# Optimization experiments

Measured on AMD Instinct MI355X. Metric: run time of the kernel, lower is better.

The kernel has to match this reference:

```python
import jax, jax.numpy as jnp
import numpy as np

N, E, ND, ED, H1, H2 = 50000, 800000, 128, 16, 256, 32
NEG_SLOPE = 0.2


def setup_inputs() -> dict:
    key = jax.random.key(0)
    ks = jax.random.split(key, 12)
    s = lambda k, shape: jax.random.normal(k, shape, jnp.float32) * 0.05
    return dict(
        x=jax.random.normal(ks[0], (N, ND), jnp.float32),
        edge_index=jax.random.randint(ks[1], (2, E), 0, N),
        edge_attr=jax.random.normal(ks[2], (E, ED), jnp.float32),
        Wl1=s(ks[3], (H1, ND)), bl1=jnp.zeros((H1,), jnp.float32),
        Wr1=s(ks[4], (H1, ND)), br1=jnp.zeros((H1,), jnp.float32),
        We1=s(ks[5], (H1, ED)), att1=s(ks[6], (H1,)), bias1=jnp.zeros((H1,), jnp.float32),
        Wl2=s(ks[7], (H2, H1)), bl2=jnp.zeros((H2,), jnp.float32),
        Wr2=s(ks[8], (H2, H1)), br2=jnp.zeros((H2,), jnp.float32),
        We2=s(ks[9], (H2, ED)), att2=s(ks[10], (H2,)), bias2=jnp.zeros((H2,), jnp.float32),
    )


def _gatv2_layer(x, src, dst, ea, Wl, bl, Wr, br, We, att, bias, n):
    # heads=1, concat=True  (PyG GATv2Conv defaults)
    xl = x @ Wl.T + bl                      # [n, C]  source transform
    xr = x @ Wr.T + br                      # [n, C]  target transform
    # per-edge message: x_j + x_i + lin_edge(edge_attr), then LeakyReLU
    m = jax.nn.leaky_relu(xl[src] + xr[dst] + ea @ We.T, NEG_SLOPE)  # [Etot, C]
    logit = m @ att                         # [Etot]
    # segment softmax over destination nodes (numerically stable)
    lmax = jax.ops.segment_max(logit, dst, num_segments=n)
    lmax = jnp.where(jnp.isfinite(lmax), lmax, 0.0)
    a = jnp.exp(logit - lmax[dst])
    denom = jax.ops.segment_sum(a, dst, num_segments=n)
    a = a / denom[dst]                      # self-loops guarantee denom > 0
    # scatter-add of alpha-weighted source features, plus output bias
    return jax.ops.segment_sum(xl[src] * a[:, None], dst, num_segments=n) + bias


def reference(x, edge_index, edge_attr,
              Wl1, bl1, Wr1, br1, We1, att1, bias1,
              Wl2, bl2, Wr2, br2, We2, att2, bias2):
    n = x.shape[0]
    src, dst = edge_index[0], edge_index[1]
    # add_self_loops=True with fill_value='mean': loop attr = mean incoming edge_attr
    deg = jax.ops.segment_sum(jnp.ones_like(dst, jnp.float32), dst, num_segments=n)
    loop_attr = jax.ops.segment_sum(edge_attr, dst, num_segments=n) / jnp.maximum(deg, 1.0)[:, None]
    loop = jnp.arange(n)
    src_f = jnp.concatenate([src, loop])
    dst_f = jnp.concatenate([dst, loop])
    ea = jnp.concatenate([edge_attr, loop_attr], axis=0)
    h = _gatv2_layer(x, src_f, dst_f, ea, Wl1, bl1, Wr1, br1, We1, att1, bias1, n)
    h = _gatv2_layer(h, src_f, dst_f, ea, Wl2, bl2, Wr2, br2, We2, att2, bias2, n)
    return h.mean(axis=0)  # [out_dim]
```

## Files before the change

kernel.cpp:

```cpp
#include <hip/hip_runtime.h>
#include <math.h>

#define N_NODES 50000
#define N_EDGES 800000
#define ND 128
#define ED 16
#define H1 256
#define H2 32

typedef short bf16x8 __attribute__((ext_vector_type(8)));
typedef float f32x4 __attribute__((ext_vector_type(4)));
typedef _Float16 half2v __attribute__((ext_vector_type(2)));

__device__ __forceinline__ float dot2h(uint a, uint b, float c) {
    asm("v_dot2_f32_f16 %0, %1, %2, %0" : "+v"(c) : "v"(a), "v"(b));
    return c;
}
__device__ __forceinline__ float fmamix_lo(uint a, float b, float c) {
    float d;
    asm("v_fma_mix_f32 %0, %1, %2, %3 op_sel_hi:[1,0,0]" : "=v"(d) : "v"(a), "v"(b), "v"(c));
    return d;
}
__device__ __forceinline__ float fmamix_hi(uint a, float b, float c) {
    float d;
    asm("v_fma_mix_f32 %0, %1, %2, %3 op_sel:[1,0,0] op_sel_hi:[1,0,0]" : "=v"(d) : "v"(a), "v"(b), "v"(c));
    return d;
}
__device__ __forceinline__ ushort f2bf(float f) {
    uint u = __float_as_uint(f);
    return (ushort)((u + 0x7fff + ((u >> 16) & 1)) >> 16);
}

__global__ void k_deg(const int* __restrict__ ei, int* __restrict__ counts, int E) {
    int e = blockIdx.x * blockDim.x + threadIdx.x;
    if (e < E) atomicAdd(&counts[ei[E + e]], 1);
}

__global__ void k_scan1(const int* __restrict__ counts, int* __restrict__ partial, int n, int chunk) {
    __shared__ int sh[256];
    int beg = blockIdx.x * chunk, end = min(beg + chunk, n);
    int sum = 0;
    for (int i = beg + threadIdx.x; i < end; i += 256) sum += counts[i] + 1;
    sh[threadIdx.x] = sum;
    __syncthreads();
    for (int off = 128; off; off >>= 1) {
        if (threadIdx.x < off) sh[threadIdx.x] += sh[threadIdx.x + off];
        __syncthreads();
    }
    if (threadIdx.x == 0) partial[blockIdx.x] = sh[0];
}
__global__ void k_scan2(int* __restrict__ partial) {
    __shared__ int sh[256];
    int v = partial[threadIdx.x];
    sh[threadIdx.x] = v;
    __syncthreads();
    for (int off = 1; off < 256; off <<= 1) {
        int t = (threadIdx.x >= off) ? sh[threadIdx.x - off] : 0;
        __syncthreads();
        sh[threadIdx.x] += t;
        __syncthreads();
    }
    partial[threadIdx.x] = sh[threadIdx.x] - v;
}
__global__ void k_scan3(const int* __restrict__ counts, const int* __restrict__ partial,
                        int* __restrict__ rowptr, int n, int chunk) {
    __shared__ int sh[256];
    int beg = blockIdx.x * chunk, end = min(beg + chunk, n);
    int run = partial[blockIdx.x];
    for (int base = beg; base < end; base += 256) {
        int i = base + threadIdx.x;
        int v = (i < end) ? counts[i] + 1 : 0;
        sh[threadIdx.x] = v;
        __syncthreads();
        for (int off = 1; off < 256; off <<= 1) {
            int t = (threadIdx.x >= off) ? sh[threadIdx.x - off] : 0;
            __syncthreads();
            sh[threadIdx.x] += t;
            __syncthreads();
        }
        if (i < end) rowptr[i + 1] = run + sh[threadIdx.x];
        __syncthreads();
        run += sh[255];
        __syncthreads();
    }
    if (blockIdx.x == 0 && threadIdx.x == 0) rowptr[0] = 0;
}

__global__ void k_fill_csr(const int* __restrict__ ei, const float* __restrict__ ea,
                           const int* __restrict__ rowptr, int* __restrict__ fill,
                           int* __restrict__ csr_src, _Float16* __restrict__ ea_h, int E, int n) {
    int idx = blockIdx.x * blockDim.x + threadIdx.x;
    if (idx < E) {
        int dst = ei[E + idx];
        int slot = rowptr[dst] + atomicAdd(&fill[dst], 1);
        csr_src[slot] = ei[idx];
        const float* srow = ea + (size_t)idx * ED;
        _Float16* drow = ea_h + (size_t)slot * ED;
        #pragma unroll
        for (int q = 0; q < 4; ++q) {
            float4 f = ((const float4*)srow)[q];
            drow[q * 4 + 0] = (_Float16)f.x;
            drow[q * 4 + 1] = (_Float16)f.y;
            drow[q * 4 + 2] = (_Float16)f.z;
            drow[q * 4 + 3] = (_Float16)f.w;
        }
    } else if (idx < E + n) {
        int i = idx - E;
        csr_src[rowptr[i + 1] - 1] = i;
    }
}

__global__ __launch_bounds__(256) void k_loop_mean(_Float16* __restrict__ ea_h,
                                                   const int* __restrict__ rowptr, int n) {
    int lane = threadIdx.x & 63;
    int wave = (blockIdx.x * blockDim.x + threadIdx.x) >> 6;
    int nwaves = (gridDim.x * blockDim.x) >> 6;
    int g = lane >> 3, q = lane & 7;
    for (int node = wave; node < n; node += nwaves) {
        int beg = rowptr[node], last = rowptr[node + 1] - 1;
        float sx = 0.f, sy = 0.f;
        for (int r = beg + g; r < last; r += 8) {
            uint v = *(const uint*)((const char*)ea_h + ((uint)r << 5) + (q << 2));
            half2v h = __builtin_bit_cast(half2v, v);
            sx += (float)h.x;
            sy += (float)h.y;
        }
        #pragma unroll
        for (int off = 8; off <= 32; off <<= 1) {
            sx += __shfl_xor(sx, off);
            sy += __shfl_xor(sy, off);
        }
        if (lane < 8) {
            int cnt = last - beg;
            float inv = 1.f / (float)(cnt > 0 ? cnt : 1);
            half2v o;
            o.x = (_Float16)(sx * inv);
            o.y = (_Float16)(sy * inv);
            *(uint*)((char*)ea_h + ((uint)last << 5) + (q << 2)) = __builtin_bit_cast(uint, o);
        }
    }
}

__global__ void k_pack_half(const float* __restrict__ src, _Float16* __restrict__ dst, int total) {
    int i = blockIdx.x * blockDim.x + threadIdx.x;
    if (i < total) dst[i] = (_Float16)src[i];
}
__global__ void k_pack_bf16x4(const float* __restrict__ src, ushort* __restrict__ dst, int total4) {
    int i = blockIdx.x * blockDim.x + threadIdx.x;
    if (i >= total4) return;
    float4 f = ((const float4*)src)[i];
    ushort4 o;
    o.x = f2bf(f.x); o.y = f2bf(f.y); o.z = f2bf(f.z); o.w = f2bf(f.w);
    ((ushort4*)dst)[i] = o;
}
__global__ void k_pack_wcat(const float* __restrict__ Wa, const float* __restrict__ Wb,
                            ushort* __restrict__ dst, int C, int K) {
    int i = blockIdx.x * blockDim.x + threadIdx.x;
    if (i >= 2 * C * K) return;
    int row = i / K, k = i - row * K;
    float v = (row < C) ? Wa[(size_t)row * K + k] : Wb[(size_t)(row - C) * K + k];
    dst[i] = f2bf(v);
}

template <int HALF_A>
__global__ __launch_bounds__(256) void k_gemm_mfma(const ushort* __restrict__ Xb,
                                                   const ushort* __restrict__ Wc,
                                                   const float* __restrict__ ba,
                                                   const float* __restrict__ bb,
                                                   void* __restrict__ Ya,
                                                   float* __restrict__ Yb,
                                                   int n, int K, int C) {
    int tid = threadIdx.x;
    int lane = tid & 63, wv = tid >> 6;
    int r = lane & 15, kg = lane >> 4;
    int row0 = blockIdx.x * 64 + wv * 16;
    int colblk = blockIdx.y * 64;
    int arow = row0 + r;
    if (arow >= n) arow = n - 1;
    const ushort* aptr = Xb + (size_t)arow * K + kg * 8;
    f32x4 acc[4] = {};
    for (int k0 = 0; k0 < K; k0 += 32) {
        bf16x8 av = *(const bf16x8*)(aptr + k0);
        #pragma unroll
        for (int t = 0; t < 4; ++t) {
            const ushort* bptr = Wc + (size_t)(colblk + t * 16 + r) * K + k0 + kg * 8;
            bf16x8 bv = *(const bf16x8*)bptr;
            acc[t] = __builtin_amdgcn_mfma_f32_16x16x32_bf16(av, bv, acc[t], 0, 0, 0);
        }
    }
    #pragma unroll
    for (int t = 0; t < 4; ++t) {
        int col = colblk + t * 16 + r;
        int rowb = row0 + kg * 4;
        #pragma unroll
        for (int q = 0; q < 4; ++q) {
            int row = rowb + q;
            if (row >= n) continue;
            float v = acc[t][q];
            if (col < C) {
                v += ba[col];
                if (HALF_A) ((_Float16*)Ya)[(size_t)row * C + col] = (_Float16)v;
                else        ((float*)Ya)[(size_t)row * C + col] = v;
            } else {
                Yb[(size_t)row * C + (col - C)] = v + bb[col - C];
            }
        }
    }
}

__device__ __forceinline__ float logit1(const uint (&w)[4][8], uint4 e0, uint4 e1,
                                        uint2 xv, float4 xrv, float4 a06, float4 a04) {
    float we[4];
    #pragma unroll
    for (int r = 0; r < 4; ++r) {
        float s = dot2h(w[r][0], e0.x, 0.f);
        s = dot2h(w[r][1], e0.y, s);
        s = dot2h(w[r][2], e0.z, s);
        s = dot2h(w[r][3], e0.w, s);
        s = dot2h(w[r][4], e1.x, s);
        s = dot2h(w[r][5], e1.y, s);
        s = dot2h(w[r][6], e1.z, s);
        s = dot2h(w[r][7], e1.w, s);
        we[r] = s;
    }
    float z0 = fmamix_lo(xv.x, 1.0f, we[0] + xrv.x);
    float z1 = fmamix_hi(xv.x, 1.0f, we[1] + xrv.y);
    float z2 = fmamix_lo(xv.y, 1.0f, we[2] + xrv.z);
    float z3 = fmamix_hi(xv.y, 1.0f, we[3] + xrv.w);
    return fmaf(a06.x, z0, fmaf(a04.x, fabsf(z0),
           fmaf(a06.y, z1, fmaf(a04.y, fabsf(z1),
           fmaf(a06.z, z2, fmaf(a04.z, fabsf(z2),
           fmaf(a06.w, z3, a04.w * fabsf(z3))))))));
}

__global__ __launch_bounds__(256) void k_gat1(const _Float16* __restrict__ xlh,
                                              const float* __restrict__ xr,
                                              const _Float16* __restrict__ ea_h,
                                              const _Float16* __restrict__ We_h,
                                              const float* __restrict__ att,
                                              const float* __restrict__ bias,
                                              const int* __restrict__ rowptr,
                                              const int* __restrict__ csr_src,
                                              ushort* __restrict__ out_bf, int n) {
    const int lane = threadIdx.x & 63;
    int wave = (blockIdx.x * blockDim.x + threadIdx.x) >> 6;
    int nwaves = (gridDim.x * blockDim.x) >> 6;
    const uint* Wp = (const uint*)We_h;
    uint w[4][8];
    #pragma unroll
    for (int r = 0; r < 4; ++r)
        #pragma unroll
        for (int q = 0; q < 8; ++q) w[r][q] = Wp[(lane * 4 + r) * 8 + q];
    float4 attv = ((const float4*)att)[lane];
    float4 bv = ((const float4*)bias)[lane];
    float4 a06, a04;
    a06.x = 0.6f * attv.x; a06.y = 0.6f * attv.y; a06.z = 0.6f * attv.z; a06.w = 0.6f * attv.w;
    a04.x = 0.4f * attv.x; a04.y = 0.4f * attv.y; a04.z = 0.4f * attv.z; a04.w = 0.4f * attv.w;
    const uint laneoff = (uint)lane << 3;

    for (int node = wave; node < n; node += nwaves) {
        float4 xrv = *(const float4*)(xr + ((size_t)node << 8) + (lane << 2));
        int beg = rowptr[node], end = rowptr[node + 1];
        float denom = 0.f, ac0 = 0.f, ac1 = 0.f, ac2 = 0.f, ac3 = 0.f;
        int j = beg;
        for (; j + 3 < end; j += 4) {
            int s0 = __builtin_amdgcn_readfirstlane(csr_src[j]);
            int s1 = __builtin_amdgcn_readfirstlane(csr_src[j + 1]);
            int s2 = __builtin_amdgcn_readfirstlane(csr_src[j + 2]);
            int s3 = __builtin_amdgcn_readfirstlane(csr_src[j + 3]);
            const uint4* eP = (const uint4*)((const char*)ea_h + ((uint)j << 5));
            uint4 e00 = eP[0], e01 = eP[1], e10 = eP[2], e11 = eP[3];
            uint4 e20 = eP[4], e21 = eP[5], e30 = eP[6], e31 = eP[7];
            uint2 x0 = *(const uint2*)((const char*)xlh + (((uint)s0 << 9) + laneoff));
            uint2 x1 = *(const uint2*)((const char*)xlh + (((uint)s1 << 9) + laneoff));
            uint2 x2 = *(const uint2*)((const char*)xlh + (((uint)s2 << 9) + laneoff));
            uint2 x3 = *(const uint2*)((const char*)xlh + (((uint)s3 << 9) + laneoff));
            float p0 = logit1(w, e00, e01, x0, xrv, a06, a04);
            float p1 = logit1(w, e10, e11, x1, xrv, a06, a04);
            float p2 = logit1(w, e20, e21, x2, xrv, a06, a04);
            float p3 = logit1(w, e30, e31, x3, xrv, a06, a04);
            #pragma unroll
            for (int off = 32; off >= 1; off >>= 1) {
                p0 += __shfl_xor(p0, off);
                p1 += __shfl_xor(p1, off);
                p2 += __shfl_xor(p2, off);
                p3 += __shfl_xor(p3, off);
            }
            float q0 = __expf(p0), q1 = __expf(p1);
            float q2 = __expf(p2), q3 = __expf(p3);
            denom += (q0 + q1) + (q2 + q3);
            ac0 = fmamix_lo(x0.x, q0, ac0); ac1 = fmamix_hi(x0.x, q0, ac1);
            ac2 = fmamix_lo(x0.y, q0, ac2); ac3 = fmamix_hi(x0.y, q0, ac3);
            ac0 = fmamix_lo(x1.x, q1, ac0); ac1 = fmamix_hi(x1.x, q1, ac1);
            ac2 = fmamix_lo(x1.y, q1, ac2); ac3 = fmamix_hi(x1.y, q1, ac3);
            ac0 = fmamix_lo(x2.x, q2, ac0); ac1 = fmamix_hi(x2.x, q2, ac1);
            ac2 = fmamix_lo(x2.y, q2, ac2); ac3 = fmamix_hi(x2.y, q2, ac3);
            ac0 = fmamix_lo(x3.x, q3, ac0); ac1 = fmamix_hi(x3.x, q3, ac1);
            ac2 = fmamix_lo(x3.y, q3, ac2); ac3 = fmamix_hi(x3.y, q3, ac3);
        }
        for (; j < end; ++j) {
            int s0 = __builtin_amdgcn_readfirstlane(csr_src[j]);
            const uint4* eP = (const uint4*)((const char*)ea_h + ((uint)j << 5));
            uint4 e00 = eP[0], e01 = eP[1];
            uint2 x0 = *(const uint2*)((const char*)xlh + (((uint)s0 << 9) + laneoff));
            float p0 = logit1(w, e00, e01, x0, xrv, a06, a04);
            #pragma unroll
            for (int off = 32; off >= 1; off >>= 1) p0 += __shfl_xor(p0, off);
            float q0 = __expf(p0);
            denom += q0;
            ac0 = fmamix_lo(x0.x, q0, ac0); ac1 = fmamix_hi(x0.x, q0, ac1);
            ac2 = fmamix_lo(x0.y, q0, ac2); ac3 = fmamix_hi(x0.y, q0, ac3);
        }
        float inv = 1.f / denom;
        ushort4 o;
        o.x = f2bf(fmaf(ac0, inv, bv.x));
        o.y = f2bf(fmaf(ac1, inv, bv.y));
        o.z = f2bf(fmaf(ac2, inv, bv.z));
        o.w = f2bf(fmaf(ac3, inv, bv.w));
        *(ushort4*)(out_bf + ((size_t)node << 8) + (lane << 2)) = o;
    }
}

__global__ __launch_bounds__(256) void k_gat2(const float* __restrict__ xl,
                                              const float* __restrict__ xr,
                                              const _Float16* __restrict__ ea_h,
                                              const _Float16* __restrict__ We_h,
                                              const float* __restrict__ att,
                                              const float* __restrict__ bias,
                                              const int* __restrict__ rowptr,
                                              const int* __restrict__ csr_src,
                                              float* __restrict__ out, int n) {
    int tid = threadIdx.x;
    int lane = tid & 63;
    int sub = lane >> 5, c = lane & 31;
    int wave = (blockIdx.x * blockDim.x + tid) >> 6;
    int nwaves = (gridDim.x * blockDim.x) >> 6;
    const uint* Wp = (const uint*)We_h;
    uint w0 = Wp[c * 8 + 0], w1 = Wp[c * 8 + 1], w2 = Wp[c * 8 + 2], w3 = Wp[c * 8 + 3];
    uint w4 = Wp[c * 8 + 4], w5 = Wp[c * 8 + 5], w6 = Wp[c * 8 + 6], w7 = Wp[c * 8 + 7];
    float attc = att[c];
    float a06 = 0.6f * attc, a04 = 0.4f * attc;
    float bc = bias[c];

    for (int node = wave; node < n; node += nwaves) {
        float xrc = xr[((size_t)node << 5) + c];
        int beg = rowptr[node], end = rowptr[node + 1];
        float denom = 0.f, acc = 0.f;
        int j = beg;
        for (; j + 3 < end; j += 4) {
            int jA = j + sub, jB = j + 2 + sub;
            int sA = csr_src[jA], sB = csr_src[jB];
            const uint4* ePA = (const uint4*)((const char*)ea_h + ((uint)jA << 5));
            const uint4* ePB = (const uint4*)((const char*)ea_h + ((uint)jB << 5));
            uint4 a0 = ePA[0], a1 = ePA[1];
            uint4 b0 = ePB[0], b1 = ePB[1];
            float xlA = *(const float*)((const char*)xl + (((uint)sA << 7) + (c << 2)));
            float xlB = *(const float*)((const char*)xl + (((uint)sB << 7) + (c << 2)));
            float weA = dot2h(w7, a1.w, dot2h(w6, a1.z, dot2h(w5, a1.y, dot2h(w4, a1.x,
                        dot2h(w3, a0.w, dot2h(w2, a0.z, dot2h(w1, a0.y, dot2h(w0, a0.x, 0.f))))))));
            float weB = dot2h(w7, b1.w, dot2h(w6, b1.z, dot2h(w5, b1.y, dot2h(w4, b1.x,
                        dot2h(w3, b0.w, dot2h(w2, b0.z, dot2h(w1, b0.y, dot2h(w0, b0.x, 0.f))))))));
            float zA = xlA + xrc + weA;
            float zB = xlB + xrc + weB;
            float pA = fmaf(a06, zA, a04 * fabsf(zA));
            float pB = fmaf(a06, zB, a04 * fabsf(zB));
            #pragma unroll
            for (int off = 16; off >= 1; off >>= 1) {
                pA += __shfl_xor(pA, off);
                pB += __shfl_xor(pB, off);
            }
            float qA = __expf(pA), qB = __expf(pB);
            denom += qA + qB;
            acc = fmaf(qA, xlA, fmaf(qB, xlB, acc));
        }
        for (; j < end; j += 2) {
            int jj = j + sub;
            bool act = jj < end;
            int js = act ? jj : j;
            int s = csr_src[js];
            const uint4* eP = (const uint4*)((const char*)ea_h + ((uint)js << 5));
            uint4 e0 = eP[0], e1 = eP[1];
            float xlv = *(const float*)((const char*)xl + (((uint)s << 7) + (c << 2)));
            float we = dot2h(w7, e1.w, dot2h(w6, e1.z, dot2h(w5, e1.y, dot2h(w4, e1.x,
                       dot2h(w3, e0.w, dot2h(w2, e0.z, dot2h(w1, e0.y, dot2h(w0, e0.x, 0.f))))))));
            float z = xlv + xrc + we;
            float p = fmaf(a06, z, a04 * fabsf(z));
            #pragma unroll
            for (int off = 16; off >= 1; off >>= 1) p += __shfl_xor(p, off);
            float pe = act ? __expf(p) : 0.f;
            denom += pe;
            acc = fmaf(pe, xlv, acc);
        }
        acc += __shfl_xor(acc, 32);
        denom += __shfl_xor(denom, 32);
        if (sub == 0) out[((size_t)node << 5) + c] = acc / denom + bc;
    }
}

__global__ __launch_bounds__(256) void k_mean(const float* __restrict__ h2,
                                              float* __restrict__ out, int total, float invN) {
    __shared__ float red[H2];
    int tid = threadIdx.x;
    if (tid < H2) red[tid] = 0.f;
    __syncthreads();
    float part = 0.f;
    for (int idx = blockIdx.x * blockDim.x + tid; idx < total; idx += gridDim.x * blockDim.x)
        part += h2[idx];
    atomicAdd(&red[tid & 31], part);
    __syncthreads();
    if (tid < H2) atomicAdd(&out[tid], red[tid] * invN);
}

extern "C" void kernel_launch(void* const* d_in, const int* in_sizes, int n_in,
                              void* d_out, int out_size, void* d_ws, size_t ws_size,
                              hipStream_t stream) {
    const float* x   = (const float*)d_in[0];
    const int*   ei  = (const int*)d_in[1];
    const float* ea  = (const float*)d_in[2];
    const float* Wl1 = (const float*)d_in[3];
    const float* bl1 = (const float*)d_in[4];
    const float* Wr1 = (const float*)d_in[5];
    const float* br1 = (const float*)d_in[6];
    const float* We1 = (const float*)d_in[7];
    const float* at1 = (const float*)d_in[8];
    const float* bi1 = (const float*)d_in[9];
    const float* Wl2 = (const float*)d_in[10];
    const float* bl2 = (const float*)d_in[11];
    const float* Wr2 = (const float*)d_in[12];
    const float* br2 = (const float*)d_in[13];
    const float* We2 = (const float*)d_in[14];
    const float* at2 = (const float*)d_in[15];
    const float* bi2 = (const float*)d_in[16];
    float* out = (float*)d_out;

    const int N = N_NODES, E = N_EDGES, ET = N_EDGES + N_NODES;
    const int SCAN_CHUNK = (N + 255) / 256;

    size_t off = 0;
    auto carve = [&](size_t bytes) {
        void* p = (char*)d_ws + off;
        off += (bytes + 255) & ~(size_t)255;
        return p;
    };
    int*      counts  = (int*)carve((size_t)N * 4);
    int*      fill    = (int*)carve((size_t)N * 4);
    int*      rowptr  = (int*)carve((size_t)(N + 1) * 4);
    int*      partial = (int*)carve(256 * 4);
    int*      csr_src = (int*)carve((size_t)ET * 4);
    _Float16* ea_h    = (_Float16*)carve((size_t)ET * ED * 2);
    _Float16* We1_h   = (_Float16*)carve((size_t)H1 * ED * 2);
    _Float16* We2_h   = (_Float16*)carve((size_t)H2 * ED * 2);
    ushort*   x_bf    = (ushort*)carve((size_t)N * ND * 2);
    ushort*   wcat1   = (ushort*)carve((size_t)2 * H1 * ND * 2);
    ushort*   wcat2   = (ushort*)carve((size_t)2 * H2 * H1 * 2);
    _Float16* xl1h    = (_Float16*)carve((size_t)N * H1 * 2);
    float*    xr1     = (float*)carve((size_t)N * H1 * 4);
    ushort*   h1_bf   = (ushort*)carve((size_t)N * H1 * 2);
    float*    xl2     = (float*)carve((size_t)N * H2 * 4);
    float*    xr2     = (float*)carve((size_t)N * H2 * 4);
    float*    h2      = (float*)carve((size_t)N * H2 * 4);

    hipMemsetAsync(counts, 0, (size_t)N * 4, stream);
    hipMemsetAsync(fill, 0, (size_t)N * 4, stream);
    hipMemsetAsync(out, 0, (size_t)H2 * 4, stream);

    k_deg<<<(E + 255) / 256, 256, 0, stream>>>(ei, counts, E);
    k_scan1<<<256, 256, 0, stream>>>(counts, partial, N, SCAN_CHUNK);
    k_scan2<<<1, 256, 0, stream>>>(partial);
    k_scan3<<<256, 256, 0, stream>>>(counts, partial, rowptr, N, SCAN_CHUNK);
    k_fill_csr<<<(E + N + 255) / 256, 256, 0, stream>>>(ei, ea, rowptr, fill, csr_src, ea_h, E, N);
    k_loop_mean<<<1024, 256, 0, stream>>>(ea_h, rowptr, N);
    k_pack_half<<<(H1 * ED + 255) / 256, 256, 0, stream>>>(We1, We1_h, H1 * ED);
    k_pack_half<<<(H2 * ED + 255) / 256, 256, 0, stream>>>(We2, We2_h, H2 * ED);
    k_pack_bf16x4<<<(N * ND / 4 + 255) / 256, 256, 0, stream>>>(x, x_bf, N * ND / 4);
    k_pack_wcat<<<(2 * H1 * ND + 255) / 256, 256, 0, stream>>>(Wl1, Wr1, wcat1, H1, ND);
    k_pack_wcat<<<(2 * H2 * H1 + 255) / 256, 256, 0, stream>>>(Wl2, Wr2, wcat2, H2, H1);

    k_gemm_mfma<1><<<dim3((N + 63) / 64, (2 * H1) / 64), 256, 0, stream>>>(
        x_bf, wcat1, bl1, br1, (void*)xl1h, xr1, N, ND, H1);
    k_gat1<<<4096, 256, 0, stream>>>(xl1h, xr1, ea_h, We1_h, at1, bi1,
                                     rowptr, csr_src, h1_bf, N);

    k_gemm_mfma<0><<<dim3((N + 63) / 64, (2 * H2) / 64), 256, 0, stream>>>(
        h1_bf, wcat2, bl2, br2, (void*)xl2, xr2, N, H1, H2);
    k_gat2<<<12500, 256, 0, stream>>>(xl2, xr2, ea_h, We2_h, at2, bi2,
                                      rowptr, csr_src, h2, N);

    k_mean<<<128, 256, 0, stream>>>(h2, out, N * H2, 1.0f / (float)N);
}
```

Measured before the change: 478.3 us.

## Scalar-load edge data in GAT layer 1, store xr in fp16, fuse pack kernels

In the layer-1 attention kernel, edge attributes and source indices shared by the whole wave now come in through scalar s_load instructions into SGPRs and feed v_dot2 directly from scalar operands. This replaces redundant per-lane vector loads. The target transform xr1 is written as fp16 instead of fp32, which halves its traffic, and the five small pack kernels plus two memsets are merged into one launch each. The inline-asm s_waitcnt serialises the scalar loads, and fp16 xr slightly lowers precision.

After: 439.5 us. 8.1% less time.

```diff
diff --git a/kernel.cpp b/kernel.cpp
--- a/kernel.cpp
+++ b/kernel.cpp
@@ -11,9 +11,15 @@
 typedef short bf16x8 __attribute__((ext_vector_type(8)));
 typedef float f32x4 __attribute__((ext_vector_type(4)));
 typedef _Float16 half2v __attribute__((ext_vector_type(2)));
-
-__device__ __forceinline__ float dot2h(uint a, uint b, float c) {
-    asm("v_dot2_f32_f16 %0, %1, %2, %0" : "+v"(c) : "v"(a), "v"(b));
+typedef uint uintx4 __attribute__((ext_vector_type(4)));
+typedef uint uintx8 __attribute__((ext_vector_type(8)));
+
+__device__ __forceinline__ float dot2h(uint w_, uint ea_v, float c) {
+    asm("v_dot2_f32_f16 %0, %1, %2, %0" : "+v"(c) : "v"(w_), "v"(ea_v));
+    return c;
+}
+__device__ __forceinline__ float dot2hs(uint w_, uint ea_s, float c) {
+    asm("v_dot2_f32_f16 %0, %2, %1, %0" : "+v"(c) : "v"(w_), "s"(ea_s));
     return c;
 }
 __device__ __forceinline__ float fmamix_lo(uint a, float b, float c) {
@@ -29,6 +35,18 @@
 __device__ __forceinline__ ushort f2bf(float f) {
     uint u = __float_as_uint(f);
     return (ushort)((u + 0x7fff + ((u >> 16) & 1)) >> 16);
+}
+__device__ __forceinline__ void sload_iter(const int* pc, const char* pe,
+                                           uintx4& c, uintx8& e0, uintx8& e1,
+                                           uintx8& e2, uintx8& e3) {
+    asm volatile("s_load_dwordx4 %0, %5, 0x0\n\t"
+                 "s_load_dwordx8 %1, %6, 0x0\n\t"
+                 "s_load_dwordx8 %2, %6, 0x20\n\t"
+                 "s_load_dwordx8 %3, %6, 0x40\n\t"
+                 "s_load_dwordx8 %4, %6, 0x60\n\t"
+                 "s_waitcnt lgkmcnt(0)"
+                 : "=s"(c), "=s"(e0), "=s"(e1), "=s"(e2), "=s"(e3)
+                 : "s"(pc), "s"(pe));
 }
 
 __global__ void k_deg(const int* __restrict__ ei, int* __restrict__ counts, int E) {
@@ -141,34 +159,54 @@
     }
 }
 
-__global__ void k_pack_half(const float* __restrict__ src, _Float16* __restrict__ dst, int total) {
-    int i = blockIdx.x * blockDim.x + threadIdx.x;
-    if (i < total) dst[i] = (_Float16)src[i];
-}
-__global__ void k_pack_bf16x4(const float* __restrict__ src, ushort* __restrict__ dst, int total4) {
-    int i = blockIdx.x * blockDim.x + threadIdx.x;
-    if (i >= total4) return;
-    float4 f = ((const float4*)src)[i];
-    ushort4 o;
-    o.x = f2bf(f.x); o.y = f2bf(f.y); o.z = f2bf(f.z); o.w = f2bf(f.w);
-    ((ushort4*)dst)[i] = o;
-}
-__global__ void k_pack_wcat(const float* __restrict__ Wa, const float* __restrict__ Wb,
-                            ushort* __restrict__ dst, int C, int K) {
-    int i = blockIdx.x * blockDim.x + threadIdx.x;
-    if (i >= 2 * C * K) return;
-    int row = i / K, k = i - row * K;
-    float v = (row < C) ? Wa[(size_t)row * K + k] : Wb[(size_t)(row - C) * K + k];
-    dst[i] = f2bf(v);
-}
-
-template <int HALF_A>
+__global__ __launch_bounds__(256) void k_pack_all(const float* __restrict__ x,
+                                                  const float* __restrict__ Wl1,
+                                                  const float* __restrict__ Wr1,
+                                                  const float* __restrict__ We1,
+                                                  const float* __restrict__ Wl2,
+                                                  const float* __restrict__ Wr2,
+                                                  const float* __restrict__ We2,
+                                                  ushort* __restrict__ x_bf,
+                                                  ushort* __restrict__ wcat1,
+                                                  ushort* __restrict__ wcat2,
+                                                  _Float16* __restrict__ We1_h,
+                                                  _Float16* __restrict__ We2_h) {
+    const int T4 = N_NODES * ND / 4;
+    int idx = blockIdx.x * blockDim.x + threadIdx.x;
+    if (idx < T4) {
+        float4 f = ((const float4*)x)[idx];
+        ushort4 o;
+        o.x = f2bf(f.x); o.y = f2bf(f.y); o.z = f2bf(f.z); o.w = f2bf(f.w);
+        ((ushort4*)x_bf)[idx] = o;
+        return;
+    }
+    int k = idx - T4;
+    if (k < 2 * H1 * ND) {
+        int row = k / ND, kk = k - row * ND;
+        float v = (row < H1) ? Wl1[(size_t)row * ND + kk] : Wr1[(size_t)(row - H1) * ND + kk];
+        wcat1[k] = f2bf(v);
+        return;
+    }
+    k -= 2 * H1 * ND;
+    if (k < 2 * H2 * H1) {
+        int row = k / H1, kk = k - row * H1;
+        float v = (row < H2) ? Wl2[(size_t)row * H1 + kk] : Wr2[(size_t)(row - H2) * H1 + kk];
+        wcat2[k] = f2bf(v);
+        return;
+    }
+    k -= 2 * H2 * H1;
+    if (k < H1 * ED) { We1_h[k] = (_Float16)We1[k]; return; }
+    k -= H1 * ED;
+    if (k < H2 * ED) We2_h[k] = (_Float16)We2[k];
+}
+
+template <int HALF_A, int HALF_B>
 __global__ __launch_bounds__(256) void k_gemm_mfma(const ushort* __restrict__ Xb,
                                                    const ushort* __restrict__ Wc,
                                                    const float* __restrict__ ba,
                                                    const float* __restrict__ bb,
                                                    void* __restrict__ Ya,
-                                                   float* __restrict__ Yb,
+                                                   void* __restrict__ Yb,
                                                    int n, int K, int C) {
     int tid = threadIdx.x;
     int lane = tid & 63, wv = tid >> 6;
@@ -202,39 +240,56 @@
                 if (HALF_A) ((_Float16*)Ya)[(size_t)row * C + col] = (_Float16)v;
                 else        ((float*)Ya)[(size_t)row * C + col] = v;
             } else {
-                Yb[(size_t)row * C + (col - C)] = v + bb[col - C];
+                v += bb[col - C];
+                if (HALF_B) ((_Float16*)Yb)[(size_t)row * C + (col - C)] = (_Float16)v;
+                else        ((float*)Yb)[(size_t)row * C + (col - C)] = v;
             }
         }
     }
 }
 
-__device__ __forceinline__ float logit1(const uint (&w)[4][8], uint4 e0, uint4 e1,
-                                        uint2 xv, float4 xrv, float4 a06, float4 a04) {
-    float we[4];
+__device__ __forceinline__ float logit_s(const uint (&w)[4][8], const uint* es,
+                                         uint2 xv, float4 xrv, float4 a06, float4 a04) {
+    float we0 = 0.f, we1 = 0.f, we2 = 0.f, we3 = 0.f;
     #pragma unroll
-    for (int r = 0; r < 4; ++r) {
-        float s = dot2h(w[r][0], e0.x, 0.f);
-        s = dot2h(w[r][1], e0.y, s);
-        s = dot2h(w[r][2], e0.z, s);
-        s = dot2h(w[r][3], e0.w, s);
-        s = dot2h(w[r][4], e1.x, s);
-        s = dot2h(w[r][5], e1.y, s);
-        s = dot2h(w[r][6], e1.z, s);
-        s = dot2h(w[r][7], e1.w, s);
-        we[r] = s;
-    }
-    float z0 = fmamix_lo(xv.x, 1.0f, we[0] + xrv.x);
-    float z1 = fmamix_hi(xv.x, 1.0f, we[1] + xrv.y);
-    float z2 = fmamix_lo(xv.y, 1.0f, we[2] + xrv.z);
-    float z3 = fmamix_hi(xv.y, 1.0f, we[3] + xrv.w);
+    for (int q = 0; q < 8; ++q) {
+        we0 = dot2hs(w[0][q], es[q], we0);
+        we1 = dot2hs(w[1][q], es[q], we1);
+        we2 = dot2hs(w[2][q], es[q], we2);
+        we3 = dot2hs(w[3][q], es[q], we3);
+    }
+    float z0 = fmamix_lo(xv.x, 1.0f, we0 + xrv.x);
+    float z1 = fmamix_hi(xv.x, 1.0f, we1 + xrv.y);
+    float z2 = fmamix_lo(xv.y, 1.0f, we2 + xrv.z);
+    float z3 = fmamix_hi(xv.y, 1.0f, we3 + xrv.w);
     return fmaf(a06.x, z0, fmaf(a04.x, fabsf(z0),
            fmaf(a06.y, z1, fmaf(a04.y, fabsf(z1),
            fmaf(a06.z, z2, fmaf(a04.z, fabsf(z2),
            fmaf(a06.w, z3, a04.w * fabsf(z3))))))));
 }
+__device__ __forceinline__ float logit_v(const uint (&w)[4][8], uint4 e0, uint4 e1,
+                                         uint2 xv, float4 xrv, float4 a06, float4 a04) {
+    uint ev[8] = {e0.x, e0.y, e0.z, e0.w, e1.x, e1.y, e1.z, e1.w};
+    float we0 = 0.f, we1 = 0.f, we2 = 0.f, we3 = 0.f;
+    #pragma unroll
+    for (int q = 0; q < 8; ++q) {
+        we0 = dot2h(w[0][q], ev[q], we0);
+        we1 = dot2h(w[1][q], ev[q], we1);
+        we2 = dot2h(w[2][q], ev[q], we2);
+        we3 = dot2h(w[3][q], ev[q], we3);
+    }
+    float z0 = fmamix_lo(xv.x, 1.0f, we0 + xrv.x);
+    float z1 = fmamix_hi(xv.x, 1.0f, we1 + xrv.y);
+    float z2 = fmamix_lo(xv.y, 1.0f, we2 + xrv.z);
+    float z3 = fmamix_hi(xv.y, 1.0f, we3 + xrv.w);
+    return fmaf(a06.x, z0, fmaf(a04.x, fabsf(z0),
+           fmaf(a06.y, z1, fmaf(a04.y, fabsf(z1),
+           fmaf(a06.z, z2, fmaf(a04.z, fabsf(z2),
+           fmaf(a06.w, z3, a04.w * fabsf(z3))))))));
+}
 
 __global__ __launch_bounds__(256) void k_gat1(const _Float16* __restrict__ xlh,
-                                              const float* __restrict__ xr,
+                                              const _Float16* __restrict__ xrh,
                                               const _Float16* __restrict__ ea_h,
                                               const _Float16* __restrict__ We_h,
                                               const float* __restrict__ att,
@@ -259,26 +314,32 @@
     const uint laneoff = (uint)lane << 3;
 
     for (int node = wave; node < n; node += nwaves) {
-        float4 xrv = *(const float4*)(xr + ((size_t)node << 8) + (lane << 2));
+        uint2 xru = *(const uint2*)((const char*)xrh + ((size_t)node << 9) + laneoff);
+        half2v xr0 = __builtin_bit_cast(half2v, xru.x);
+        half2v xr1 = __builtin_bit_cast(half2v, xru.y);
+        float4 xrv;
+        xrv.x = (float)xr0.x; xrv.y = (float)xr0.y;
+        xrv.z = (float)xr1.x; xrv.w = (float)xr1.y;
         int beg = rowptr[node], end = rowptr[node + 1];
         float denom = 0.f, ac0 = 0.f, ac1 = 0.f, ac2 = 0.f, ac3 = 0.f;
         int j = beg;
         for (; j + 3 < end; j += 4) {
-            int s0 = __builtin_amdgcn_readfirstlane(csr_src[j]);
-            int s1 = __builtin_amdgcn_readfirstlane(csr_src[j + 1]);
-            int s2 = __builtin_amdgcn_readfirstlane(csr_src[j + 2]);
-            int s3 = __builtin_amdgcn_readfirstlane(csr_src[j + 3]);
-            const uint4* eP = (const uint4*)((const char*)ea_h + ((uint)j << 5));
-            uint4 e00 = eP[0], e01 = eP[1], e10 = eP[2], e11 = eP[3];
-            uint4 e20 = eP[4], e21 = eP[5], e30 = eP[6], e31 = eP[7];
-            uint2 x0 = *(const uint2*)((const char*)xlh + (((uint)s0 << 9) + laneoff));
-            uint2 x1 = *(const uint2*)((const char*)xlh + (((uint)s1 << 9) + laneoff));
-            uint2 x2 = *(const uint2*)((const char*)xlh + (((uint)s2 << 9) + laneoff));
-            uint2 x3 = *(const uint2*)((const char*)xlh + (((uint)s3 << 9) + laneoff));
-            float p0 = logit1(w, e00, e01, x0, xrv, a06, a04);
-            float p1 = logit1(w, e10, e11, x1, xrv, a06, a04);
-            float p2 = logit1(w, e20, e21, x2, xrv, a06, a04);
-            float p3 = logit1(w, e30, e31, x3, xrv, a06, a04);
+            int ju = __builtin_amdgcn_readfirstlane(j);
+            uintx4 cs;
+            uintx8 ea0, ea1, ea2, ea3;
+            sload_iter(csr_src + ju, (const char*)ea_h + ((size_t)ju << 5), cs, ea0, ea1, ea2, ea3);
+            uint s0 = cs[0], s1 = cs[1], s2 = cs[2], s3 = cs[3];
+            uint2 x0 = *(const uint2*)((const char*)xlh + ((size_t)s0 << 9) + laneoff);
+            uint2 x1 = *(const uint2*)((const char*)xlh + ((size_t)s1 << 9) + laneoff);
+            uint2 x2 = *(const uint2*)((const char*)xlh + ((size_t)s2 << 9) + laneoff);
+            uint2 x3 = *(const uint2*)((const char*)xlh + ((size_t)s3 << 9) + laneoff);
+            uint eA[8], eB[8], eC[8], eD[8];
+            #pragma unroll
+            for (int q = 0; q < 8; ++q) { eA[q] = ea0[q]; eB[q] = ea1[q]; eC[q] = ea2[q]; eD[q] = ea3[q]; }
+            float p0 = logit_s(w, eA, x0, xrv, a06, a04);
+            float p1 = logit_s(w, eB, x1, xrv, a06, a04);
+            float p2 = logit_s(w, eC, x2, xrv, a06, a04);
+            float p3 = logit_s(w, eD, x3, xrv, a06, a04);
             #pragma unroll
             for (int off = 32; off >= 1; off >>= 1) {
                 p0 += __shfl_xor(p0, off);
@@ -300,10 +361,10 @@
         }
         for (; j < end; ++j) {
             int s0 = __builtin_amdgcn_readfirstlane(csr_src[j]);
-            const uint4* eP = (const uint4*)((const char*)ea_h + ((uint)j << 5));
+            const uint4* eP = (const uint4*)((const char*)ea_h + ((size_t)(uint)j << 5));
             uint4 e00 = eP[0], e01 = eP[1];
-            uint2 x0 = *(const uint2*)((const char*)xlh + (((uint)s0 << 9) + laneoff));
-            float p0 = logit1(w, e00, e01, x0, xrv, a06, a04);
+            uint2 x0 = *(const uint2*)((const char*)xlh + ((size_t)(uint)s0 << 9) + laneoff);
+            float p0 = logit_v(w, e00, e01, x0, xrv, a06, a04);
             #pragma unroll
             for (int off = 32; off >= 1; off >>= 1) p0 += __shfl_xor(p0, off);
             float q0 = __expf(p0);
@@ -454,14 +515,14 @@
     ushort*   wcat1   = (ushort*)carve((size_t)2 * H1 * ND * 2);
     ushort*   wcat2   = (ushort*)carve((size_t)2 * H2 * H1 * 2);
     _Float16* xl1h    = (_Float16*)carve((size_t)N * H1 * 2);
-    float*    xr1     = (float*)carve((size_t)N * H1 * 4);
+    _Float16* xr1h    = (_Float16*)carve((size_t)N * H1 * 2);
     ushort*   h1_bf   = (ushort*)carve((size_t)N * H1 * 2);
     float*    xl2     = (float*)carve((size_t)N * H2 * 4);
     float*    xr2     = (float*)carve((size_t)N * H2 * 4);
     float*    h2      = (float*)carve((size_t)N * H2 * 4);
 
-    hipMemsetAsync(counts, 0, (size_t)N * 4, stream);
-    hipMemsetAsync(fill, 0, (size_t)N * 4, stream);
+    size_t zspan = (size_t)((char*)fill - (char*)counts) + (size_t)N * 4;
+    hipMemsetAsync(counts, 0, zspan, stream);
     hipMemsetAsync(out, 0, (size_t)H2 * 4, stream);
 
     k_deg<<<(E + 255) / 256, 256, 0, stream>>>(ei, counts, E);
@@ -470,19 +531,19 @@
     k_scan3<<<256, 256, 0, stream>>>(counts, partial, rowptr, N, SCAN_CHUNK);
     k_fill_csr<<<(E + N + 255) / 256, 256, 0, stream>>>(ei, ea, rowptr, fill, csr_src, ea_h, E, N);
     k_loop_mean<<<1024, 256, 0, stream>>>(ea_h, rowptr, N);
-    k_pack_half<<<(H1 * ED + 255) / 256, 256, 0, stream>>>(We1, We1_h, H1 * ED);
-    k_pack_half<<<(H2 * ED + 255) / 256, 256, 0, stream>>>(We2, We2_h, H2 * ED);
-    k_pack_bf16x4<<<(N * ND / 4 + 255) / 256, 256, 0, stream>>>(x, x_bf, N * ND / 4);
-    k_pack_wcat<<<(2 * H1 * ND + 255) / 256, 256, 0, stream>>>(Wl1, Wr1, wcat1, H1, ND);
-    k_pack_wcat<<<(2 * H2 * H1 + 255) / 256, 256, 0, stream>>>(Wl2, Wr2, wcat2, H2, H1);
-
-    k_gemm_mfma<1><<<dim3((N + 63) / 64, (2 * H1) / 64), 256, 0, stream>>>(
-        x_bf, wcat1, bl1, br1, (void*)xl1h, xr1, N, ND, H1);
-    k_gat1<<<4096, 256, 0, stream>>>(xl1h, xr1, ea_h, We1_h, at1, bi1,
+
+    const int T4 = N_NODES * ND / 4;
+    const int TS = 2 * H1 * ND + 2 * H2 * H1 + H1 * ED + H2 * ED;
+    k_pack_all<<<(T4 + TS + 255) / 256, 256, 0, stream>>>(x, Wl1, Wr1, We1, Wl2, Wr2, We2,
+                                                          x_bf, wcat1, wcat2, We1_h, We2_h);
+
+    k_gemm_mfma<1, 1><<<dim3((N + 63) / 64, (2 * H1) / 64), 256, 0, stream>>>(
+        x_bf, wcat1, bl1, br1, (void*)xl1h, (void*)xr1h, N, ND, H1);
+    k_gat1<<<4096, 256, 0, stream>>>(xl1h, xr1h, ea_h, We1_h, at1, bi1,
                                      rowptr, csr_src, h1_bf, N);
 
-    k_gemm_mfma<0><<<dim3((N + 63) / 64, (2 * H2) / 64), 256, 0, stream>>>(
-        h1_bf, wcat2, bl2, br2, (void*)xl2, xr2, N, H1, H2);
+    k_gemm_mfma<0, 0><<<dim3((N + 63) / 64, (2 * H2) / 64), 256, 0, stream>>>(
+        h1_bf, wcat2, bl2, br2, (void*)xl2, (void*)xr2, N, H1, H2);
     k_gat2<<<12500, 256, 0, stream>>>(xl2, xr2, ea_h, We2_h, at2, bi2,
                                       rowptr, csr_src, h2, N);
 
```
